# Performance work log

Hardware: AMD Instinct MI355X
Metric: run time of the kernel (lower is better)

Reference implementation:

```python
import jax, jax.numpy as jnp
import numpy as np

XB = (-51.2, 51.2, 0.8); YB = (-51.2, 51.2, 0.8); ZB = (-10.0, 10.0, 20.0); DB = (4.0, 45.0, 1.0)
H_FEAT, W_FEAT = 16, 44
C_IN, C_OUT = 512, 64
D = int((DB[1] - DB[0]) / DB[2])  # 41
DX = np.array([XB[2], YB[2], ZB[2]], np.float32)
BX = np.array([XB[0] + XB[2] / 2.0, YB[0] + YB[2] / 2.0, ZB[0] + ZB[2] / 2.0], np.float32)
NX0 = int((XB[1] - XB[0]) / XB[2])  # 128
NX1 = int((YB[1] - YB[0]) / YB[2])  # 128
NX2 = int((ZB[1] - ZB[0]) / ZB[2])  # 1
NVOX = NX0 * NX1 * NX2


def _frustum():
    ds = np.arange(DB[0], DB[1], DB[2], dtype=np.float32)[:, None, None]
    xs = np.linspace(0, W_FEAT - 1, W_FEAT, dtype=np.float32)[None, None, :]
    ys = np.linspace(0, H_FEAT - 1, H_FEAT, dtype=np.float32)[None, :, None]
    shape = (D, H_FEAT, W_FEAT)
    return jnp.asarray(np.stack([np.broadcast_to(xs, shape), np.broadcast_to(ys, shape), np.broadcast_to(ds, shape)], -1))


def setup_inputs() -> dict:
    rng = np.random.default_rng(0)
    B, N = 4, 6
    img_feats = rng.standard_normal((B, N, C_IN, H_FEAT, W_FEAT)).astype(np.float32)
    depth_w = (0.02 * rng.standard_normal((D + C_OUT, C_IN))).astype(np.float32)
    depth_b = np.zeros((D + C_OUT,), np.float32)
    ang = rng.uniform(-np.pi, np.pi, (B, N))
    c, s = np.cos(ang), np.sin(ang)
    rots = np.zeros((B, N, 3, 3), np.float32)
    rots[..., 0, 0] = c; rots[..., 0, 1] = -s
    rots[..., 1, 0] = s; rots[..., 1, 1] = c
    rots[..., 2, 2] = 1.0
    trans = rng.uniform(-2.0, 2.0, (B, N, 3)).astype(np.float32)
    trans[..., 2] *= 0.25
    intr = np.array([[20.0, 0.0, 22.0], [0.0, 20.0, 8.0], [0.0, 0.0, 1.0]], np.float32)
    intrins = np.broadcast_to(intr, (B, N, 3, 3)).copy()
    post_rots = np.broadcast_to(np.eye(3, dtype=np.float32), (B, N, 3, 3)).copy()
    post_trans = np.zeros((B, N, 3), np.float32)
    return {k: jnp.asarray(v) for k, v in dict(img_feats=img_feats, depth_w=depth_w, depth_b=depth_b, rots=rots, trans=trans, intrins=intrins, post_rots=post_rots, post_trans=post_trans).items()}


def reference(img_feats, depth_w, depth_b, rots, trans, intrins, post_rots, post_trans):
    B, N = img_feats.shape[:2]
    # depth net: 1x1 conv == channel matmul
    xf = img_feats.reshape(B * N, C_IN, H_FEAT, W_FEAT)
    feat = jnp.einsum('bchw,oc->bohw', xf, depth_w) + depth_b[None, :, None, None]
    depth = jax.nn.softmax(feat[:, :D], axis=1)      # (BN, D, H, W)
    tran = feat[:, D:]                               # (BN, C, H, W)
    # lift: outer product over depth x channel
    outer = depth[:, None, :, :, :] * tran[:, :, None, :, :]          # (BN, C, D, H, W)
    feats = outer.reshape(B, N, C_OUT, D, H_FEAT, W_FEAT).transpose(0, 1, 3, 4, 5, 2)  # (B,N,D,H,W,C)
    # geometry
    pts = _frustum()[None, None] - post_trans[:, :, None, None, None, :]
    pts = jnp.einsum('bnij,bndhwj->bndhwi', jnp.linalg.inv(post_rots), pts)
    pts = jnp.concatenate([pts[..., :2] * pts[..., 2:3], pts[..., 2:3]], axis=-1)
    combine = rots @ jnp.linalg.inv(intrins)
    pts = jnp.einsum('bnij,bndhwj->bndhwi', combine, pts) + trans[:, :, None, None, None, :]
    # voxelize; int cast truncates toward zero, matching torch .long()
    coords = ((pts - jnp.asarray(BX)) / jnp.asarray(DX)).astype(jnp.int32)  # (B,N,D,H,W,3)
    cx, cy, cz = coords[..., 0], coords[..., 1], coords[..., 2]
    valid = (cx >= 0) & (cx < NX0) & (cy >= 0) & (cy < NX1) & (cz >= 0) & (cz < NX2)
    ranks = jnp.where(valid, cx + cy * NX0 + cz * (NX0 * NX1), NVOX)  # invalid -> dropped bin
    sums = jax.ops.segment_sum(feats.reshape(-1, C_OUT), ranks.reshape(-1), num_segments=NVOX + 1)
    bev = sums[:NVOX].reshape(NX2, NX1, NX0, C_OUT).sum(0)            # (ny, nx, C)
    return jnp.transpose(bev, (2, 0, 1))[None]                        # (1, C, ny, nx)
```

## Files before the change

kernel.cpp:

```cpp
#include <hip/hip_runtime.h>
#include <cmath>

#define CIN   512
#define COUT  64
#define DBINS 41
#define NFEAT 105
#define HF    16
#define WF    44
#define NPIX  704
#define NCAM  24
#define NXG   128
#define NVOX  16384
#define ROWF  210
#define BEVOF 146
#define NPAIR (NCAM * NPIX * DBINS)
#define NSUB  16
#define NCNT  (NVOX * NSUB)


#define WS_BSUM  5120
#define WS_BBASE 6144
#define WS_FEAT  8192
#define WS_OFFS  14200832
#define WS_REC   15249408
#define WS_CNT   15249408

__device__ __forceinline__ void inv3(const double a[9], double o[9]) {
    double c00 =  a[4]*a[8] - a[5]*a[7];
    double c01 = -(a[3]*a[8] - a[5]*a[6]);
    double c02 =  a[3]*a[7] - a[4]*a[6];
    double det = a[0]*c00 + a[1]*c01 + a[2]*c02;
    double id  = 1.0 / det;
    o[0] = c00 * id;
    o[1] = -(a[1]*a[8] - a[2]*a[7]) * id;
    o[2] =  (a[1]*a[5] - a[2]*a[4]) * id;
    o[3] = c01 * id;
    o[4] =  (a[0]*a[8] - a[2]*a[6]) * id;
    o[5] = -(a[0]*a[5] - a[2]*a[3]) * id;
    o[6] = c02 * id;
    o[7] = -(a[0]*a[7] - a[1]*a[6]) * id;
    o[8] =  (a[0]*a[4] - a[1]*a[3]) * id;
}

__global__ __launch_bounds__(64) void setup_zero_k(const float* __restrict__ rots,
                                                   const float* __restrict__ trans,
                                                   const float* __restrict__ intrins,
                                                   const float* __restrict__ post_rots,
                                                   const float* __restrict__ post_trans,
                                                   double* __restrict__ cams,
                                                   int* __restrict__ cnt16) {
    int base = (blockIdx.x * 64 + threadIdx.x) * 16;
    int4 z = make_int4(0, 0, 0, 0);
    #pragma unroll
    for (int j = 0; j < 4; ++j)
        *reinterpret_cast<int4*>(&cnt16[base + j * 4]) = z;

    if (blockIdx.x == 0 && threadIdx.x < NCAM) {
        int i = threadIdx.x;
        double R[9], K[9], PR[9], Kinv[9], PRinv[9];
        for (int k = 0; k < 9; ++k) {
            R[k]  = (double)rots[i*9 + k];
            K[k]  = (double)intrins[i*9 + k];
            PR[k] = (double)post_rots[i*9 + k];
        }
        inv3(K, Kinv);
        inv3(PR, PRinv);
        double* o = cams + (size_t)i * 24;
        for (int k = 0; k < 9; ++k) o[k] = PRinv[k];
        o[9]  = (double)post_trans[i*3 + 0];
        o[10] = (double)post_trans[i*3 + 1];
        o[11] = (double)post_trans[i*3 + 2];
        for (int r = 0; r < 3; ++r)
            for (int c = 0; c < 3; ++c)
                o[12 + r*3 + c] = R[r*3+0]*Kinv[0*3+c] + R[r*3+1]*Kinv[1*3+c] + R[r*3+2]*Kinv[2*3+c];
        o[21] = (double)trans[i*3 + 0];
        o[22] = (double)trans[i*3 + 1];
        o[23] = (double)trans[i*3 + 2];
    }
}

__global__ __launch_bounds__(256) void gemm_feat_k(const float* __restrict__ x,
                                                   const float* __restrict__ w,
                                                   const float* __restrict__ bias,
                                                   float* __restrict__ feat) {
    __shared__ float smem[4096];

    int bx   = blockIdx.x;
    int kh   = bx & 1;
    int oh   = (bx >> 1) % 7;
    int tile = (bx >> 1) / 7;
    int p0g  = tile * 128;
    int lane = threadIdx.x & 63;
    int wid  = threadIdx.x >> 6;
    int obase0 = (oh < 6) ? oh * 16 : 89;

    int og = obase0 + wid * 4;
    const float* wbase = w + (size_t)__builtin_amdgcn_readfirstlane(og) * CIN + kh * 256;

    int spx  = threadIdx.x & 127;
    int skq  = threadIdx.x >> 7;
    int gpix = p0g + spx;
    int sbn  = gpix / NPIX;
    int sp   = gpix - sbn * NPIX;
    const float* gx = x + ((size_t)sbn * CIN + kh * 256) * NPIX + sp;

    float xr[2][4];
    float acc[4][2];
    #pragma unroll
    for (int i = 0; i < 4; ++i)
        #pragma unroll
        for (int j = 0; j < 2; ++j) acc[i][j] = 0.0f;

    #pragma unroll
    for (int q = 0; q < 2; ++q)
        #pragma unroll
        for (int c = 0; c < 4; ++c)
            xr[q][c] = gx[(size_t)((skq + 2 * q) * 4 + c) * NPIX];
    #pragma unroll
    for (int q = 0; q < 2; ++q)
        *reinterpret_cast<float4*>(&smem[((skq + 2 * q) * 128 + spx) * 4]) =
            make_float4(xr[q][0], xr[q][1], xr[q][2], xr[q][3]);
    #pragma unroll
    for (int q = 0; q < 2; ++q)
        #pragma unroll
        for (int c = 0; c < 4; ++c)
            xr[q][c] = gx[(size_t)(16 + (skq + 2 * q) * 4 + c) * NPIX];
    __syncthreads();

    #pragma unroll 1
    for (int kt = 0; kt < 16; ++kt) {
        int cur = kt & 1;
        if (kt < 15) {
            float* xsn = smem + (cur ^ 1) * 2048;
            #pragma unroll
            for (int q = 0; q < 2; ++q)
                *reinterpret_cast<float4*>(&xsn[((skq + 2 * q) * 128 + spx) * 4]) =
                    make_float4(xr[q][0], xr[q][1], xr[q][2], xr[q][3]);
        }
        if (kt < 14) {
            #pragma unroll
            for (int q = 0; q < 2; ++q)
                #pragma unroll
                for (int c = 0; c < 4; ++c)
                    xr[q][c] = gx[(size_t)((kt + 2) * 16 + (skq + 2 * q) * 4 + c) * NPIX];
        }
        const float* xs = smem + cur * 2048;
        const float* wk = wbase + kt * 16;
        #pragma unroll
        for (int kq = 0; kq < 4; ++kq) {
            float4 xv[2];
            #pragma unroll
            for (int j = 0; j < 2; ++j)
                xv[j] = *reinterpret_cast<const float4*>(&xs[(kq * 128 + lane + j * 64) * 4]);
            #pragma unroll
            for (int i = 0; i < 4; ++i) {
                float4 wv = *reinterpret_cast<const float4*>(wk + (size_t)i * CIN + (kq << 2));
                #pragma unroll
                for (int j = 0; j < 2; ++j) {
                    acc[i][j] = fmaf(xv[j].x, wv.x, acc[i][j]);
                    acc[i][j] = fmaf(xv[j].y, wv.y, acc[i][j]);
                    acc[i][j] = fmaf(xv[j].z, wv.z, acc[i][j]);
                    acc[i][j] = fmaf(xv[j].w, wv.w, acc[i][j]);
                }
            }
        }
        __syncthreads();
    }

    float* ep = smem;
    #pragma unroll
    for (int i = 0; i < 4; ++i) {
        int o = obase0 + wid * 4 + i;
        float b = (kh == 0) ? bias[o] : 0.0f;
        #pragma unroll
        for (int j = 0; j < 2; ++j)
            ep[(lane + j * 64) * 17 + wid * 4 + i] = acc[i][j] + b;
    }
    __syncthreads();
    for (int idx = threadIdx.x; idx < 128 * 16; idx += 256) {
        int px = idx >> 4;
        int ol = idx & 15;
        feat[(size_t)(p0g + px) * ROWF + kh * NFEAT + obase0 + ol] = ep[px * 17 + ol];
    }
}

__global__ __launch_bounds__(256) void phaseA_k(float* __restrict__ feat,
                                                const double* __restrict__ cams,
                                                int* __restrict__ cnt16) {
    int wid  = threadIdx.x >> 6;
    int lane = threadIdx.x & 63;
    int pix  = blockIdx.x * 4 + wid;
    int bn   = pix / NPIX;
    int p    = pix - bn * NPIX;
    int h    = p / WF;
    int wpx  = p - h * WF;

    __shared__ float f[4][NFEAT];
    float* row = feat + (size_t)pix * ROWF;
    for (int o = lane; o < NFEAT; o += 64) f[wid][o] = row[o] + row[NFEAT + o];
    __syncthreads();

    float v = (lane < DBINS) ? f[wid][lane] : -1e30f;
    float m = v;
    #pragma unroll
    for (int o = 32; o > 0; o >>= 1) m = fmaxf(m, __shfl_xor(m, o, 64));
    float e = (lane < DBINS) ? expf(v - m) : 0.0f;
    float s = e;
    #pragma unroll
    for (int o = 32; o > 0; o >>= 1) s += __shfl_xor(s, o, 64);

    int   rk = -1;
    float pd = 0.0f;
    if (lane < DBINS) {
        pd = e / s;
        const double* cm = cams + (size_t)bn * 24;
        double dd = 4.0 + (double)lane;
        double ax = (double)wpx - cm[9];
        double ay = (double)h   - cm[10];
        double az = dd          - cm[11];
        double q0 = cm[0]*ax + cm[1]*ay + cm[2]*az;
        double q1 = cm[3]*ax + cm[4]*ay + cm[5]*az;
        double q2 = cm[6]*ax + cm[7]*ay + cm[8]*az;
        double r0 = q0 * q2, r1 = q1 * q2, r2 = q2;
        double sx = cm[12]*r0 + cm[13]*r1 + cm[14]*r2 + cm[21];
        double sy = cm[15]*r0 + cm[16]*r1 + cm[17]*r2 + cm[22];
        double sz = cm[18]*r0 + cm[19]*r1 + cm[20]*r2 + cm[23];
        int cx = (int)((sx + 50.8) / 0.8);
        int cy = (int)((sy + 50.8) / 0.8);
        int cz = (int)(sz / 20.0);
        bool ok = (cx >= 0) && (cx < NXG) && (cy >= 0) && (cy < NXG) && (cz == 0);
        rk = ok ? (cy * NXG + cx) : -1;
    }
    int  rkprev = __shfl_up(rk, 1, 64);
    bool head   = (rk >= 0) && (lane == 0 || rk != rkprev);

    if (lane < DBINS) {
        row[64 + lane] = pd;
        ((int*)row)[105 + lane] = rk;
    }
    if (head) atomicAdd(&cnt16[(pix & 15) * NVOX + rk], 1);
    row[lane] = f[wid][DBINS + lane];
    row[BEVOF + lane] = 0.0f;
}

__device__ __forceinline__ int physidx(int l) { return (l & 15) * NVOX + (l >> 4); }

__global__ __launch_bounds__(256) void scan1_k(const int* __restrict__ cnt,
                                               int* __restrict__ bsum) {
    __shared__ int sc[256];
    int t = threadIdx.x;
    int base = blockIdx.x * 1024 + t * 4;
    int s = 0;
    #pragma unroll
    for (int j = 0; j < 4; ++j) s += cnt[physidx(base + j)];
    sc[t] = s;
    __syncthreads();
    for (int off = 128; off > 0; off >>= 1) {
        if (t < off) sc[t] += sc[t + off];
        __syncthreads();
    }
    if (t == 0) bsum[blockIdx.x] = sc[0];
}

__global__ __launch_bounds__(256) void scan2_k(const int* __restrict__ bsum,
                                               int* __restrict__ bbase) {
    __shared__ int sc[256];
    int t = threadIdx.x;
    int v = bsum[t];
    sc[t] = v;
    __syncthreads();
    for (int off = 1; off < 256; off <<= 1) {
        int a = (t >= off) ? sc[t - off] : 0;
        __syncthreads();
        sc[t] += a;
        __syncthreads();
    }
    bbase[t] = sc[t] - v;
}

__global__ __launch_bounds__(256) void scan3_k(const int* __restrict__ cnt,
                                               const int* __restrict__ bbase,
                                               int* __restrict__ offs) {
    __shared__ int sc[256];
    int t = threadIdx.x;
    int base = blockIdx.x * 1024 + t * 4;
    int loc[4];
    int s = 0;
    #pragma unroll
    for (int j = 0; j < 4; ++j) { loc[j] = cnt[physidx(base + j)]; s += loc[j]; }
    sc[t] = s;
    __syncthreads();
    for (int off = 1; off < 256; off <<= 1) {
        int a = (t >= off) ? sc[t - off] : 0;
        __syncthreads();
        sc[t] += a;
        __syncthreads();
    }
    int run = bbase[blockIdx.x] + sc[t] - s;
    #pragma unroll
    for (int j = 0; j < 4; ++j) { offs[physidx(base + j)] = run; run += loc[j]; }
}

__global__ __launch_bounds__(256) void place_k(float* __restrict__ feat,
                                               int* __restrict__ offs16,
                                               unsigned* __restrict__ rec) {
    int i = blockIdx.x * 256 + threadIdx.x;
    if (i >= NPAIR) return;
    int pix = i / DBINS;
    int d   = i - pix * DBINS;
    float* row = feat + (size_t)pix * ROWF;
    const int* rowI = (const int*)row;
    int r = rowI[105 + d];
    if (r < 0) return;
    if (d > 0 && rowI[105 + d - 1] == r) return;
    float wsum = row[64 + d];
    for (int j = d + 1; j < DBINS && rowI[105 + j] == r; ++j)
        wsum += row[64 + j];
    row[64 + d] = wsum;
    int pos = atomicAdd(&offs16[(pix & 15) * NVOX + r], 1);
    rec[pos] = ((unsigned)pix << 6) | (unsigned)d;
}

__global__ __launch_bounds__(256) void combine_k(float* __restrict__ feat,
                                                 const int* __restrict__ offs16,
                                                 const unsigned* __restrict__ rec) {
    int ncnt = offs16[NCNT - 1];
    int lane = threadIdx.x & 63;
    int wave = (blockIdx.x << 2) + (threadIdx.x >> 6);
    int nwav = gridDim.x << 2;
    int nchunk = (ncnt + 31) >> 5;

    for (int ch = wave; ch < nchunk; ch += nwav) {
        int i0 = ch << 5;
        int n  = min(32, ncnt - i0);
        int   rv = -1, pv = 0;
        float wv = 0.0f;
        if (lane < n) {
            unsigned e = rec[i0 + lane];
            pv = (int)(e >> 6);
            int d = (int)(e & 63u);
            const float* row = feat + (size_t)pv * ROWF;
            rv = ((const int*)row)[105 + d];
            wv = row[64 + d];
        }
        float acc = 0.0f;
        if (n == 32) {
            float xv[32];
            #pragma unroll
            for (int j = 0; j < 32; ++j) {
                int pj = __shfl(pv, j, 64);
                xv[j] = feat[(size_t)pj * ROWF + lane];
            }
            #pragma unroll
            for (int j = 0; j < 32; ++j) {
                int   rj = __shfl(rv, j, 64);
                float wj = __shfl(wv, j, 64);
                acc = fmaf(wj, xv[j], acc);
                int rn = __shfl(rv, (j + 1) & 31, 64);
                if (j == 31 || rn != rj) {
                    atomicAdd(&feat[(size_t)rj * ROWF + BEVOF + lane], acc);
                    acc = 0.0f;
                }
            }
        } else {
            for (int j = 0; j < n; ++j) {
                int   rj = __shfl(rv, j, 64);
                float wj = __shfl(wv, j, 64);
                int   pj = __shfl(pv, j, 64);
                acc = fmaf(wj, feat[(size_t)pj * ROWF + lane], acc);
                int rn = __shfl(rv, (j + 1) & 31, 64);
                if (j == n - 1 || rn != rj) {
                    atomicAdd(&feat[(size_t)rj * ROWF + BEVOF + lane], acc);
                    acc = 0.0f;
                }
            }
        }
    }
}

__global__ __launch_bounds__(256) void transpose_k(const float* __restrict__ feat,
                                                   float* __restrict__ out) {
    __shared__ float t[64][65];
    int r0 = blockIdx.x * 64;
    int c  = threadIdx.x & 63;
    int r4 = threadIdx.x >> 6;
    #pragma unroll
    for (int i = 0; i < 16; ++i) {
        int r = r4 + i * 4;
        t[r][c] = feat[(size_t)(r0 + r) * ROWF + BEVOF + c];
    }
    __syncthreads();
    int rl  = threadIdx.x & 63;
    int cc0 = threadIdx.x >> 6;
    #pragma unroll
    for (int i = 0; i < 16; ++i) {
        int ch = cc0 + i * 4;
        out[(size_t)ch * NVOX + r0 + rl] = t[rl][ch];
    }
}

extern "C" void kernel_launch(void* const* d_in, const int* in_sizes, int n_in,
                              void* d_out, int out_size, void* d_ws, size_t ws_size,
                              hipStream_t stream) {
    const float* img   = (const float*)d_in[0];
    const float* dw    = (const float*)d_in[1];
    const float* db    = (const float*)d_in[2];
    const float* rots  = (const float*)d_in[3];
    const float* trans = (const float*)d_in[4];
    const float* intr  = (const float*)d_in[5];
    const float* prot  = (const float*)d_in[6];
    const float* ptrn  = (const float*)d_in[7];
    float* out = (float*)d_out;

    char* ws = (char*)d_ws;
    double*   cams   = (double*)ws;
    int*      bsum   = (int*)(ws + WS_BSUM);
    int*      bbase  = (int*)(ws + WS_BBASE);
    float*    feat   = (float*)(ws + WS_FEAT);
    int*      offs16 = (int*)(ws + WS_OFFS);
    unsigned* rec    = (unsigned*)(ws + WS_REC);
    int*      cnt16  = (int*)(ws + WS_CNT);

    setup_zero_k<<<256, 64, 0, stream>>>(rots, trans, intr, prot, ptrn, cams, cnt16);
    gemm_feat_k<<<1848, 256, 0, stream>>>(img, dw, db, feat);
    phaseA_k<<<NCAM * NPIX / 4, 256, 0, stream>>>(feat, cams, cnt16);
    scan1_k<<<256, 256, 0, stream>>>(cnt16, bsum);
    scan2_k<<<1, 256, 0, stream>>>(bsum, bbase);
    scan3_k<<<256, 256, 0, stream>>>(cnt16, bbase, offs16);
    place_k<<<(NPAIR + 255) / 256, 256, 0, stream>>>(feat, offs16, rec);
    combine_k<<<3072, 256, 0, stream>>>(feat, offs16, rec);
    transpose_k<<<NVOX / 64, 256, 0, stream>>>(feat, out);
}
```

Measured before the change: 109.2 us.

## Move BEV accumulator to dense buffer and fuse block-sum scan into scan3

BEV accumulation moves out of the strided 210-float feature rows into a dense 64-channel buffer, which the setup kernel zeroes. This should make the atomic adds and the final transpose reads more contiguous. The single-block scan2 kernel is removed: each scan3 block now recomputes the 256-entry block-sum prefix itself, saving one launch at the cost of redundant work. It also needs extra workspace and wider zeroing at setup.

Result: no change. 108.1 us (-1.0%).

```diff
diff --git a/kernel.cpp b/kernel.cpp
--- a/kernel.cpp
+++ b/kernel.cpp
@@ -12,18 +12,17 @@
 #define NXG   128
 #define NVOX  16384
 #define ROWF  210
-#define BEVOF 146
 #define NPAIR (NCAM * NPIX * DBINS)
 #define NSUB  16
 #define NCNT  (NVOX * NSUB)
 
 
 #define WS_BSUM  5120
-#define WS_BBASE 6144
 #define WS_FEAT  8192
 #define WS_OFFS  14200832
 #define WS_REC   15249408
 #define WS_CNT   15249408
+#define WS_BEV   18020352
 
 __device__ __forceinline__ void inv3(const double a[9], double o[9]) {
     double c00 =  a[4]*a[8] - a[5]*a[7];
@@ -42,18 +41,26 @@
     o[8] =  (a[0]*a[4] - a[1]*a[3]) * id;
 }
 
-__global__ __launch_bounds__(64) void setup_zero_k(const float* __restrict__ rots,
-                                                   const float* __restrict__ trans,
-                                                   const float* __restrict__ intrins,
-                                                   const float* __restrict__ post_rots,
-                                                   const float* __restrict__ post_trans,
-                                                   double* __restrict__ cams,
-                                                   int* __restrict__ cnt16) {
-    int base = (blockIdx.x * 64 + threadIdx.x) * 16;
+__global__ __launch_bounds__(256) void setup_zero_k(const float* __restrict__ rots,
+                                                    const float* __restrict__ trans,
+                                                    const float* __restrict__ intrins,
+                                                    const float* __restrict__ post_rots,
+                                                    const float* __restrict__ post_trans,
+                                                    double* __restrict__ cams,
+                                                    int* __restrict__ cnt16,
+                                                    float* __restrict__ bev) {
     int4 z = make_int4(0, 0, 0, 0);
-    #pragma unroll
-    for (int j = 0; j < 4; ++j)
-        *reinterpret_cast<int4*>(&cnt16[base + j * 4]) = z;
+    if (blockIdx.x < 64) {
+        int base = (blockIdx.x * 256 + threadIdx.x) * 16;
+        #pragma unroll
+        for (int j = 0; j < 4; ++j)
+            *reinterpret_cast<int4*>(&cnt16[base + j * 4]) = z;
+    } else {
+        int base = ((blockIdx.x - 64) * 256 + threadIdx.x) * 16;
+        #pragma unroll
+        for (int j = 0; j < 4; ++j)
+            *reinterpret_cast<int4*>(&bev[base + j * 4]) = z;
+    }
 
     if (blockIdx.x == 0 && threadIdx.x < NCAM) {
         int i = threadIdx.x;
@@ -240,7 +247,6 @@
     }
     if (head) atomicAdd(&cnt16[(pix & 15) * NVOX + rk], 1);
     row[lane] = f[wid][DBINS + lane];
-    row[BEVOF + lane] = 0.0f;
 }
 
 __device__ __forceinline__ int physidx(int l) { return (l & 15) * NVOX + (l >> 4); }
@@ -262,27 +268,22 @@
     if (t == 0) bsum[blockIdx.x] = sc[0];
 }
 
-__global__ __launch_bounds__(256) void scan2_k(const int* __restrict__ bsum,
-                                               int* __restrict__ bbase) {
+__global__ __launch_bounds__(256) void scan3_k(const int* __restrict__ cnt,
+                                               const int* __restrict__ bsum,
+                                               int* __restrict__ offs) {
+    __shared__ int sb[256];
     __shared__ int sc[256];
     int t = threadIdx.x;
-    int v = bsum[t];
-    sc[t] = v;
+    sb[t] = bsum[t];
     __syncthreads();
     for (int off = 1; off < 256; off <<= 1) {
-        int a = (t >= off) ? sc[t - off] : 0;
-        __syncthreads();
-        sc[t] += a;
-        __syncthreads();
-    }
-    bbase[t] = sc[t] - v;
-}
-
-__global__ __launch_bounds__(256) void scan3_k(const int* __restrict__ cnt,
-                                               const int* __restrict__ bbase,
-                                               int* __restrict__ offs) {
-    __shared__ int sc[256];
-    int t = threadIdx.x;
+        int a = (t >= off) ? sb[t - off] : 0;
+        __syncthreads();
+        sb[t] += a;
+        __syncthreads();
+    }
+    int bbase = sb[blockIdx.x] - bsum[blockIdx.x];
+
     int base = blockIdx.x * 1024 + t * 4;
     int loc[4];
     int s = 0;
@@ -296,7 +297,7 @@
         sc[t] += a;
         __syncthreads();
     }
-    int run = bbase[blockIdx.x] + sc[t] - s;
+    int run = bbase + sc[t] - s;
     #pragma unroll
     for (int j = 0; j < 4; ++j) { offs[physidx(base + j)] = run; run += loc[j]; }
 }
@@ -321,9 +322,10 @@
     rec[pos] = ((unsigned)pix << 6) | (unsigned)d;
 }
 
-__global__ __launch_bounds__(256) void combine_k(float* __restrict__ feat,
+__global__ __launch_bounds__(256) void combine_k(const float* __restrict__ feat,
                                                  const int* __restrict__ offs16,
-                                                 const unsigned* __restrict__ rec) {
+                                                 const unsigned* __restrict__ rec,
+                                                 float* __restrict__ bev) {
     int ncnt = offs16[NCNT - 1];
     int lane = threadIdx.x & 63;
     int wave = (blockIdx.x << 2) + (threadIdx.x >> 6);
@@ -358,7 +360,7 @@
                 acc = fmaf(wj, xv[j], acc);
                 int rn = __shfl(rv, (j + 1) & 31, 64);
                 if (j == 31 || rn != rj) {
-                    atomicAdd(&feat[(size_t)rj * ROWF + BEVOF + lane], acc);
+                    atomicAdd(&bev[(size_t)rj * COUT + lane], acc);
                     acc = 0.0f;
                 }
             }
@@ -370,7 +372,7 @@
                 acc = fmaf(wj, feat[(size_t)pj * ROWF + lane], acc);
                 int rn = __shfl(rv, (j + 1) & 31, 64);
                 if (j == n - 1 || rn != rj) {
-                    atomicAdd(&feat[(size_t)rj * ROWF + BEVOF + lane], acc);
+                    atomicAdd(&bev[(size_t)rj * COUT + lane], acc);
                     acc = 0.0f;
                 }
             }
@@ -378,7 +380,7 @@
     }
 }
 
-__global__ __launch_bounds__(256) void transpose_k(const float* __restrict__ feat,
+__global__ __launch_bounds__(256) void transpose_k(const float* __restrict__ bev,
                                                    float* __restrict__ out) {
     __shared__ float t[64][65];
     int r0 = blockIdx.x * 64;
@@ -387,7 +389,7 @@
     #pragma unroll
     for (int i = 0; i < 16; ++i) {
         int r = r4 + i * 4;
-        t[r][c] = feat[(size_t)(r0 + r) * ROWF + BEVOF + c];
+        t[r][c] = bev[(size_t)(r0 + r) * COUT + c];
     }
     __syncthreads();
     int rl  = threadIdx.x & 63;
@@ -415,19 +417,18 @@
     char* ws = (char*)d_ws;
     double*   cams   = (double*)ws;
     int*      bsum   = (int*)(ws + WS_BSUM);
-    int*      bbase  = (int*)(ws + WS_BBASE);
     float*    feat   = (float*)(ws + WS_FEAT);
     int*      offs16 = (int*)(ws + WS_OFFS);
     unsigned* rec    = (unsigned*)(ws + WS_REC);
     int*      cnt16  = (int*)(ws + WS_CNT);
-
-    setup_zero_k<<<256, 64, 0, stream>>>(rots, trans, intr, prot, ptrn, cams, cnt16);
+    float*    bev    = (float*)(ws + WS_BEV);
+
+    setup_zero_k<<<320, 256, 0, stream>>>(rots, trans, intr, prot, ptrn, cams, cnt16, bev);
     gemm_feat_k<<<1848, 256, 0, stream>>>(img, dw, db, feat);
     phaseA_k<<<NCAM * NPIX / 4, 256, 0, stream>>>(feat, cams, cnt16);
     scan1_k<<<256, 256, 0, stream>>>(cnt16, bsum);
-    scan2_k<<<1, 256, 0, stream>>>(bsum, bbase);
-    scan3_k<<<256, 256, 0, stream>>>(cnt16, bbase, offs16);
+    scan3_k<<<256, 256, 0, stream>>>(cnt16, bsum, offs16);
     place_k<<<(NPAIR + 255) / 256, 256, 0, stream>>>(feat, offs16, rec);
-    combine_k<<<3072, 256, 0, stream>>>(feat, offs16, rec);
-    transpose_k<<<NVOX / 64, 256, 0, stream>>>(feat, out);
-}
+    combine_k<<<3072, 256, 0, stream>>>(feat, offs16, rec, bev);
+    transpose_k<<<NVOX / 64, 256, 0, stream>>>(bev, out);
+}
```
